# Performance work log

Measured on AMD Instinct MI355X. Metric: run time of the kernel, lower is better.

The kernel has to match this reference:

```python
import jax, jax.numpy as jnp
import numpy as np

CS = 64          # chunk_size
CP = CS - 1      # causal_padding
H = 8            # heads
DH = 64          # dim_head
SCALE = DH ** -0.5


def rotate_half(x):
    x1, x2 = jnp.split(x, 2, axis=-1)
    return jnp.concatenate((-x2, x1), axis=-1)


def apply_rope(t, freqs):
    rd = freqs.shape[-1]
    t_rot, t_pass = t[..., :rd], t[..., rd:]
    t_rot = t_rot * jnp.cos(freqs) + rotate_half(t_rot) * jnp.sin(freqs)
    return jnp.concatenate((t_rot, t_pass), axis=-1)


def setup_inputs() -> dict:
    key = jax.random.key(0)
    ks = jax.random.split(key, 10)
    b, n, dim = 4, 4096, 1024
    k_chunks, r, rlen = 64, 2, 128
    inner = H * DH
    return {
        "x": jax.random.normal(ks[0], (b, n, dim), dtype=jnp.float32),
        "context": jax.random.normal(ks[1], (b, k_chunks, r, rlen, dim), dtype=jnp.float32),
        "q_pos_emb": jax.random.normal(ks[2], (1, 1, CS, DH), dtype=jnp.float32),
        "k_pos_emb": jax.random.normal(ks[3], (1, 1, rlen, DH), dtype=jnp.float32),
        "Wq": jax.random.normal(ks[4], (dim, inner), dtype=jnp.float32) * 0.02,
        "Wk": jax.random.normal(ks[5], (dim, inner), dtype=jnp.float32) * 0.02,
        "Wv": jax.random.normal(ks[6], (dim, inner), dtype=jnp.float32) * 0.02,
        "Wo": jax.random.normal(ks[7], (inner, dim), dtype=jnp.float32) * 0.02,
        "bo": jnp.zeros((dim,), dtype=jnp.float32),
        "null_k": jax.random.normal(ks[8], (inner,), dtype=jnp.float32),
        "null_v": jax.random.normal(ks[9], (inner,), dtype=jnp.float32),
    }


def reference(x, context, q_pos_emb, k_pos_emb, Wq, Wk, Wv, Wo, bo, null_k, null_v):
    b, n, dim = x.shape
    _, k_chunks, r, rlen, _ = context.shape
    # causal shift: drop first CP tokens, pad CP zeros at end (F.pad with -CP)
    xs = jnp.pad(x[:, CP:], ((0, 0), (0, CP), (0, 0)))
    seq_index = (n // CS) * CS
    rem = n - seq_index
    xs = xs[:, :seq_index]                                   # [b, k*CS, dim]
    # shift q rope the same way; pad region gets freqs=0 -> identity rotation
    qpe = jnp.pad(q_pos_emb[:, :, CP:], ((0, 0), (0, 0), (0, CP), (0, 0)))
    kpe = jnp.tile(k_pos_emb, (1, 1, r, 1))                  # [1,1,r*rlen,DH]
    bk = b * k_chunks
    xc = xs.reshape(bk, CS, dim)
    ctx = context.reshape(bk, r * rlen, dim)
    # projections -> [bk, h, seq, dh]
    q = (xc @ Wq).reshape(bk, CS, H, DH).transpose(0, 2, 1, 3) * SCALE
    k = (ctx @ Wk).reshape(bk, r * rlen, H, DH).transpose(0, 2, 1, 3)
    v = (ctx @ Wv).reshape(bk, r * rlen, H, DH).transpose(0, 2, 1, 3)
    q = apply_rope(q, qpe)
    k = apply_rope(k, kpe)
    # null kv prepend
    nk = jnp.broadcast_to(null_k.reshape(1, H, 1, DH), (bk, H, 1, DH))
    nv = jnp.broadcast_to(null_v.reshape(1, H, 1, DH), (bk, H, 1, DH))
    k = jnp.concatenate((nk, k), axis=2)
    v = jnp.concatenate((nv, v), axis=2)
    sim = jnp.einsum('bhid,bhjd->bhij', q, k)
    attn = jax.nn.softmax(sim, axis=-1)
    o = jnp.einsum('bhij,bhjd->bhid', attn, v)
    o = o.transpose(0, 2, 1, 3).reshape(bk, CS, H * DH)
    o = o @ Wo + bo                                          # [bk, CS, dim]
    o = o.reshape(b, k_chunks * CS, dim)
    # unshift: pad CP zeros at front, trim CP - rem from end
    o = jnp.concatenate(
        (jnp.zeros((b, CP, dim), o.dtype), o[:, :k_chunks * CS - CP + rem]), axis=1)
    return o
```

## Files before the change

kernel.cpp:

```cpp
#include <hip/hip_runtime.h>


#define DEV __device__ __forceinline__

typedef __bf16 bf16x8 __attribute__((ext_vector_type(8)));
typedef float f32x4 __attribute__((ext_vector_type(4)));

DEV unsigned short f2bf(float f) {
  union { float f; unsigned int u; } v; v.f = f;
  unsigned int u = v.u;
  unsigned int r = (u + 0x7FFFu + ((u >> 16) & 1u)) >> 16;
  return (unsigned short)r;
}
DEV float bf2f(unsigned short h) {
  union { unsigned int u; float f; } v; v.u = ((unsigned int)h) << 16;
  return v.f;
}
DEV unsigned int pkbf(unsigned int hi, unsigned int lo) {
  return __builtin_amdgcn_perm(hi, lo, 0x07060302u);
}

DEV void ldst16(const void* g, void* l) {
  __builtin_amdgcn_global_load_lds(
      (const __attribute__((address_space(1))) void*)g,
      (__attribute__((address_space(3))) void*)l, 16, 0, 0);
}

__global__ __launch_bounds__(256) void prep_k(const float* __restrict__ Wq,
                                              const float* __restrict__ Wk,
                                              const float* __restrict__ Wv,
                                              const float* __restrict__ Wo,
                                              const float* __restrict__ qpe,
                                              const float* __restrict__ kpe,
                                              unsigned short* __restrict__ Wqt,
                                              unsigned short* __restrict__ Wkt,
                                              unsigned short* __restrict__ Wvt,
                                              unsigned short* __restrict__ Wot,
                                              float* __restrict__ ck, float* __restrict__ sk,
                                              float* __restrict__ cq, float* __restrict__ sq,
                                              float* __restrict__ out) {
  int blk = blockIdx.x;
  if (blk < 8192) {
    int idx = blk * 256 + threadIdx.x;
    int which = idx >> 19;
    int loc = idx & 524287;
    if (which < 3) {
      int k = loc & 1023, n = loc >> 10;
      const float* W = which == 0 ? Wq : (which == 1 ? Wk : Wv);
      unsigned short* Wt = which == 0 ? Wqt : (which == 1 ? Wkt : Wvt);
      float scale = which == 0 ? 0.125f : 1.0f;
      Wt[loc] = f2bf(W[(size_t)k * 512 + n] * scale);
    } else {
      int k = loc & 511, n = loc >> 9;
      Wot[loc] = f2bf(Wo[(size_t)k * 1024 + n]);
    }
  } else if (blk < 8444) {
    int r = blk - 8192;
    int b = r / 63, rr = r % 63;
    float4 z = {0.f, 0.f, 0.f, 0.f};
    *(float4*)(out + (((size_t)(b * 4096 + rr)) << 10) + threadIdx.x * 4) = z;
  } else {
    int t = (blk - 8444) * 256 + threadIdx.x;
    float f = kpe[t];
    ck[t] = cosf(f);
    sk[t] = sinf(f);
    if (t < 64) {
      float g = qpe[63 * 64 + t];
      cq[t] = cosf(g);
      sq[t] = sinf(g);
    }
  }
}

template <int MODE>
__global__ __launch_bounds__(256) void gemm_proj(const float* __restrict__ Af,
                                                 const unsigned short* __restrict__ B0,
                                                 const unsigned short* __restrict__ B1,
                                                 unsigned short* __restrict__ out0,
                                                 unsigned short* __restrict__ out1,
                                                 const float* __restrict__ ck,
                                                 const float* __restrict__ sk,
                                                 const float* __restrict__ cq,
                                                 const float* __restrict__ sq) {
  __shared__ unsigned short sh[16384];
  unsigned short* As = sh;
  unsigned short* Bs = sh + 8192;
  const int K = 1024;

  int id = blockIdx.x;
  int x, y, z;
  if (MODE == 0) { x = (id & 7) + 8 * (id >> 5); y = (id >> 3) & 3; z = 0; }
  else           { x = (id & 7) + 8 * (id >> 6); int j = (id >> 3) & 7; y = j & 3; z = j >> 2; }
  const unsigned short* B = z ? B1 : B0;
  int m0 = x * 128, n0 = y * 128;
  int tid = threadIdx.x, w = tid >> 6, lane = tid & 63;
  int wm = (w & 1) * 64, wn = (w >> 1) * 64;
  int Lrow = lane >> 3, Lc = lane & 7;
  int srcC = Lc ^ (Lrow & 7);

  const float* asrc[4];
  bool avalid[4];
  #pragma unroll
  for (int q = 0; q < 4; ++q) {
    int t = w * 4 + q;
    int gm = m0 + t * 8 + Lrow;
    if (MODE == 0) {
      int b = gm >> 12, p = gm & 4095;
      avalid[q] = (p <= 4032);
      asrc[q] = Af + (((size_t)(b << 12) + p + 63) << 10) + srcC * 8;
    } else {
      avalid[q] = true;
      asrc[q] = Af + (size_t)gm * 1024 + srcC * 8;
    }
  }

  f32x4 acc[4][4] = {};

  for (int k0 = 0; k0 < K; k0 += 64) {
    #pragma unroll
    for (int q = 0; q < 4; ++q) {
      int t = w * 4 + q;
      uint4 lo = {0, 0, 0, 0}, hi = {0, 0, 0, 0};
      if (avalid[q]) {
        lo = *(const uint4*)(asrc[q] + k0);
        hi = *(const uint4*)(asrc[q] + k0 + 4);
      }
      uint4 pk;
      pk.x = pkbf(lo.y, lo.x);
      pk.y = pkbf(lo.w, lo.z);
      pk.z = pkbf(hi.y, hi.x);
      pk.w = pkbf(hi.w, hi.z);
      *(uint4*)((char*)As + t * 1024 + lane * 16) = pk;
      ldst16(B + (size_t)(n0 + t * 8 + Lrow) * K + (k0 + srcC * 8), (char*)Bs + t * 1024);
    }
    __syncthreads();
    #pragma unroll
    for (int k32 = 0; k32 < 2; ++k32) {
      int c = k32 * 4 + (lane >> 4);
      bf16x8 af[4], bfr[4];
      #pragma unroll
      for (int mt = 0; mt < 4; ++mt) {
        int m = wm + mt * 16 + (lane & 15);
        af[mt] = *(const bf16x8*)((const char*)As + m * 128 + (c ^ (m & 7)) * 16);
      }
      #pragma unroll
      for (int nt = 0; nt < 4; ++nt) {
        int n = wn + nt * 16 + (lane & 15);
        bfr[nt] = *(const bf16x8*)((const char*)Bs + n * 128 + (c ^ (n & 7)) * 16);
      }
      #pragma unroll
      for (int mt = 0; mt < 4; ++mt)
        #pragma unroll
        for (int nt = 0; nt < 4; ++nt)
          acc[mt][nt] = __builtin_amdgcn_mfma_f32_16x16x32_bf16(af[mt], bfr[nt], acc[mt][nt], 0, 0, 0);
    }
    __syncthreads();
  }

  if (MODE == 0) {
    #pragma unroll
    for (int mt = 0; mt < 4; ++mt)
      #pragma unroll
      for (int nt = 0; nt < 4; ++nt)
        #pragma unroll
        for (int r = 0; r < 4; ++r) {
          int m = m0 + wm + mt * 16 + (lane >> 4) * 4 + r;
          int n = n0 + wn + nt * 16 + (lane & 15);
          float val = acc[mt][nt][r];
          if ((m & 63) == 0) {
            int d = nt * 16 + (lane & 15);
            float partner = acc[mt][nt ^ 2][r];
            val = val * cq[d] + (nt < 2 ? -partner : partner) * sq[d];
          }
          out0[(size_t)m * 512 + n] = f2bf(val);
        }
  } else if (z == 0) {
    #pragma unroll
    for (int mt = 0; mt < 4; ++mt)
      #pragma unroll
      for (int r = 0; r < 4; ++r) {
        int m = m0 + wm + mt * 16 + (lane >> 4) * 4 + r;
        int fib = (m & 127) * 64;
        #pragma unroll
        for (int nt = 0; nt < 4; ++nt) {
          int n = n0 + wn + nt * 16 + (lane & 15);
          int d = nt * 16 + (lane & 15);
          float partner = acc[mt][nt ^ 2][r];
          float val = acc[mt][nt][r] * ck[fib + d] + (nt < 2 ? -partner : partner) * sk[fib + d];
          out0[(size_t)m * 512 + n] = f2bf(val);
        }
      }
  } else {
    #pragma unroll
    for (int mt = 0; mt < 4; ++mt)
      #pragma unroll
      for (int nt = 0; nt < 4; ++nt)
        #pragma unroll
        for (int r = 0; r < 4; ++r) {
          int ml = wm + mt * 16 + (lane >> 4) * 4 + r;
          int nl = wn + nt * 16 + (lane & 15);
          int mc = ml >> 3, me = ml & 7;
          *(unsigned short*)((char*)sh + nl * 256 + ((mc ^ (nl & 15)) * 16) + me * 2) =
              f2bf(acc[mt][nt][r]);
        }
    __syncthreads();
    #pragma unroll
    for (int i = 0; i < 8; ++i) {
      int flat = i * 256 + tid;
      int nl = flat >> 4, mc = flat & 15;
      uint4 v = *(const uint4*)((const char*)sh + nl * 256 + ((mc ^ (nl & 15)) * 16));
      *(uint4*)(out1 + (size_t)(n0 + nl) * 65536 + m0 + mc * 8) = v;
    }
  }
}

__global__ __launch_bounds__(256) void gemm_out(const unsigned short* __restrict__ A,
                                                const unsigned short* __restrict__ B,
                                                const float* __restrict__ bias,
                                                float* __restrict__ out) {
  __shared__ unsigned short sh[16384];
  unsigned short* As = sh;
  unsigned short* Bs = sh + 8192;
  const int K = 512, N = 1024;
  int id = blockIdx.x;
  int x = (id & 7) + 8 * (id >> 6), y = (id >> 3) & 7;
  int m0 = x * 128, n0 = y * 128;
  int tid = threadIdx.x, w = tid >> 6, lane = tid & 63;
  int wm = (w & 1) * 64, wn = (w >> 1) * 64;
  int Lrow = lane >> 3, Lc = lane & 7;
  int srcC = Lc ^ (Lrow & 7);

  f32x4 acc[4][4] = {};

  for (int k0 = 0; k0 < K; k0 += 64) {
    #pragma unroll
    for (int q = 0; q < 4; ++q) {
      int t = w * 4 + q;
      ldst16(A + (size_t)(m0 + t * 8 + Lrow) * K + (k0 + srcC * 8), (char*)As + t * 1024);
      ldst16(B + (size_t)(n0 + t * 8 + Lrow) * K + (k0 + srcC * 8), (char*)Bs + t * 1024);
    }
    __syncthreads();
    #pragma unroll
    for (int k32 = 0; k32 < 2; ++k32) {
      int c = k32 * 4 + (lane >> 4);
      bf16x8 af[4], bfr[4];
      #pragma unroll
      for (int mt = 0; mt < 4; ++mt) {
        int m = wm + mt * 16 + (lane & 15);
        af[mt] = *(const bf16x8*)((const char*)As + m * 128 + (c ^ (m & 7)) * 16);
      }
      #pragma unroll
      for (int nt = 0; nt < 4; ++nt) {
        int n = wn + nt * 16 + (lane & 15);
        bfr[nt] = *(const bf16x8*)((const char*)Bs + n * 128 + (c ^ (n & 7)) * 16);
      }
      #pragma unroll
      for (int mt = 0; mt < 4; ++mt)
        #pragma unroll
        for (int nt = 0; nt < 4; ++nt)
          acc[mt][nt] = __builtin_amdgcn_mfma_f32_16x16x32_bf16(af[mt], bfr[nt], acc[mt][nt], 0, 0, 0);
    }
    __syncthreads();
  }
  #pragma unroll
  for (int mt = 0; mt < 4; ++mt)
    #pragma unroll
    for (int nt = 0; nt < 4; ++nt)
      #pragma unroll
      for (int r = 0; r < 4; ++r) {
        int m = m0 + wm + mt * 16 + (lane >> 4) * 4 + r;
        int n = n0 + wn + nt * 16 + (lane & 15);
        int b = m >> 12, t = m & 4095;
        if (t <= 4032)
          out[((size_t)((b << 12) + t + 63)) * N + n] = acc[mt][nt][r] + bias[n];
      }
}

__global__ __launch_bounds__(256) void attn_kernel(const unsigned short* __restrict__ qb,
                                                   const unsigned short* __restrict__ kb,
                                                   const unsigned short* __restrict__ vtg,
                                                   const float* __restrict__ nullk,
                                                   const float* __restrict__ nullv,
                                                   unsigned short* __restrict__ ob) {
  __shared__ unsigned short qs[64 * 64];
  __shared__ unsigned short ks[256 * 64];
  __shared__ unsigned short ps[64 * 256];
  __shared__ float rnull[64];
  __shared__ float rsum[64];
  int id = blockIdx.x;
  int bc = (id & 7) + 8 * (id >> 6);
  int h = (id >> 3) & 7;
  int tid = threadIdx.x, w = tid >> 6, lane = tid & 63;
  int Lrow = lane >> 3, Lc = lane & 7, srcC = Lc ^ (Lrow & 7);

  #pragma unroll
  for (int q8 = 0; q8 < 2; ++q8) {
    int t = w * 2 + q8;
    ldst16(qb + (size_t)(bc * 64 + t * 8 + Lrow) * 512 + h * 64 + srcC * 8, (char*)qs + t * 1024);
  }
  #pragma unroll
  for (int q8 = 0; q8 < 8; ++q8) {
    int t = w * 8 + q8;
    ldst16(kb + (size_t)(bc * 256 + t * 8 + Lrow) * 512 + h * 64 + srcC * 8, (char*)ks + t * 1024);
  }
  __syncthreads();

  {
    int rl = lane >> 2, part = lane & 3;
    int row = w * 16 + rl;
    float s = 0.f;
    #pragma unroll
    for (int e = 0; e < 16; ++e) {
      int d = part * 16 + e;
      unsigned short qv = *(const unsigned short*)((const char*)qs + row * 128 +
                                                   (((d >> 3) ^ (row & 7)) * 16) + (d & 7) * 2);
      s += bf2f(qv) * nullk[h * 64 + d];
    }
    s += __shfl_xor(s, 1);
    s += __shfl_xor(s, 2);
    if (part == 0) rnull[row] = __expf(s);
  }

  f32x4 acc[16] = {};
  #pragma unroll
  for (int k32 = 0; k32 < 2; ++k32) {
    int c = k32 * 4 + (lane >> 4);
    int m = w * 16 + (lane & 15);
    bf16x8 a = *(const bf16x8*)((const char*)qs + m * 128 + (c ^ (m & 7)) * 16);
    #pragma unroll
    for (int nt = 0; nt < 16; ++nt) {
      int n = nt * 16 + (lane & 15);
      bf16x8 b = *(const bf16x8*)((const char*)ks + n * 128 + (c ^ (n & 7)) * 16);
      acc[nt] = __builtin_amdgcn_mfma_f32_16x16x32_bf16(a, b, acc[nt], 0, 0, 0);
    }
  }

  int g = lane >> 4;
  #pragma unroll
  for (int r = 0; r < 4; ++r) {
    int row = w * 16 + g * 4 + r;
    float s = 0.f;
    #pragma unroll
    for (int nt = 0; nt < 16; ++nt) {
      float p = __expf(acc[nt][r]);
      acc[nt][r] = p;
      s += p;
    }
    s += __shfl_xor(s, 1);
    s += __shfl_xor(s, 2);
    s += __shfl_xor(s, 4);
    s += __shfl_xor(s, 8);
    if ((lane & 15) == 0) rsum[row] = s + rnull[row];
  }

  #pragma unroll
  for (int nt = 0; nt < 16; ++nt)
    #pragma unroll
    for (int r = 0; r < 4; ++r) {
      int row = w * 16 + g * 4 + r;
      int col = nt * 16 + (lane & 15);
      *(unsigned short*)((char*)ps + row * 512 + (((col >> 3) ^ (row & 7)) * 16) + (col & 7) * 2) =
          f2bf(acc[nt][r]);
    }
  __syncthreads();

  #pragma unroll
  for (int q8 = 0; q8 < 8; ++q8) {
    int t = w * 8 + q8;
    int dd = t * 2 + (lane >> 5);
    int cl = (lane & 31) ^ (dd & 7);
    ldst16(vtg + (size_t)(h * 64 + dd) * 65536 + bc * 256 + cl * 8, (char*)ks + t * 1024);
  }
  __syncthreads();

  f32x4 oacc[4] = {};
  #pragma unroll
  for (int k32 = 0; k32 < 8; ++k32) {
    int c = k32 * 4 + (lane >> 4);
    int m = w * 16 + (lane & 15);
    bf16x8 a = *(const bf16x8*)((const char*)ps + m * 512 + (c ^ (m & 7)) * 16);
    #pragma unroll
    for (int nt = 0; nt < 4; ++nt) {
      int n = nt * 16 + (lane & 15);
      bf16x8 b = *(const bf16x8*)((const char*)ks + n * 512 + (c ^ (n & 7)) * 16);
      oacc[nt] = __builtin_amdgcn_mfma_f32_16x16x32_bf16(a, b, oacc[nt], 0, 0, 0);
    }
  }
  #pragma unroll
  for (int nt = 0; nt < 4; ++nt)
    #pragma unroll
    for (int r = 0; r < 4; ++r) {
      int row = w * 16 + g * 4 + r;
      int d = nt * 16 + (lane & 15);
      float o = oacc[nt][r] + rnull[row] * nullv[h * 64 + d];
      o /= rsum[row];
      ob[((size_t)(bc * 64 + row) * 8 + h) * 64 + d] = f2bf(o);
    }
}

extern "C" void kernel_launch(void* const* d_in, const int* in_sizes, int n_in,
                              void* d_out, int out_size, void* d_ws, size_t ws_size,
                              hipStream_t stream) {
  const float* x = (const float*)d_in[0];
  const float* ctx = (const float*)d_in[1];
  const float* qpe = (const float*)d_in[2];
  const float* kpe = (const float*)d_in[3];
  const float* Wq = (const float*)d_in[4];
  const float* Wk = (const float*)d_in[5];
  const float* Wv = (const float*)d_in[6];
  const float* Wo = (const float*)d_in[7];
  const float* bo = (const float*)d_in[8];
  const float* nk = (const float*)d_in[9];
  const float* nv = (const float*)d_in[10];
  float* out = (float*)d_out;
  char* ws = (char*)d_ws;

  unsigned short* Wqt  = (unsigned short*)(ws + 0);
  unsigned short* Wkt  = (unsigned short*)(ws + 1048576);
  unsigned short* Wvt  = (unsigned short*)(ws + 2097152);
  unsigned short* Wot  = (unsigned short*)(ws + 3145728);
  unsigned short* qb   = (unsigned short*)(ws + 4194304);
  unsigned short* kb   = (unsigned short*)(ws + 20971520);
  unsigned short* vtg  = (unsigned short*)(ws + 88080384);
  unsigned short* obuf = (unsigned short*)(ws + 155189248);
  float* cosk = (float*)(ws + 171966464);
  float* sink = (float*)(ws + 171999232);
  float* cosq = (float*)(ws + 172032000);
  float* sinq = (float*)(ws + 172032256);

  prep_k<<<8476, 256, 0, stream>>>(Wq, Wk, Wv, Wo, qpe, kpe, Wqt, Wkt, Wvt, Wot,
                                   cosk, sink, cosq, sinq, out);

  gemm_proj<0><<<512, 256, 0, stream>>>(x, Wqt, Wqt, qb, nullptr,
                                        cosk, sink, cosq, sinq);
  gemm_proj<1><<<4096, 256, 0, stream>>>(ctx, Wkt, Wvt, kb, vtg,
                                         cosk, sink, cosq, sinq);

  attn_kernel<<<2048, 256, 0, stream>>>(qb, kb, vtg, nk, nv, obuf);

  gemm_out<<<1024, 256, 0, stream>>>(obuf, Wot, bo, out);
}
```

Before: 763.5 us.

## Add pipelined 256x256 KV projection GEMM and tiled weight transpose

Replaces the KV projection launch with a new gemm_kv kernel. It uses 512 threads and 256x256 tiles, double-buffered LDS, and register-staged fp32-to-bf16 conversion of the context input. Asynchronous global-to-LDS loads of B are interleaved with MFMA phases under explicit barriers, waitcnts and setprio. Separately, the weight transpose in prep_k now goes through a 64x64 shared-memory tile so both reads and writes are coalesced. The pipeline adds barrier overhead and a large LDS footprint, which limits occupancy.

```diff
diff --git a/kernel.cpp b/kernel.cpp
--- a/kernel.cpp
+++ b/kernel.cpp
@@ -25,6 +25,11 @@
       (const __attribute__((address_space(1))) void*)g,
       (__attribute__((address_space(3))) void*)l, 16, 0, 0);
 }
+
+DEV void bar() { __builtin_amdgcn_s_barrier(); }
+#define LGKM0 asm volatile("s_waitcnt lgkmcnt(0)" ::: "memory")
+#define VMCNT4 asm volatile("s_waitcnt vmcnt(4)" ::: "memory")
+#define VMCNT0 asm volatile("s_waitcnt vmcnt(0)" ::: "memory")
 
 __global__ __launch_bounds__(256) void prep_k(const float* __restrict__ Wq,
                                               const float* __restrict__ Wk,
@@ -39,28 +44,42 @@
                                               float* __restrict__ ck, float* __restrict__ sk,
                                               float* __restrict__ cq, float* __restrict__ sq,
                                               float* __restrict__ out) {
+  __shared__ float tl[64][65];
   int blk = blockIdx.x;
-  if (blk < 8192) {
-    int idx = blk * 256 + threadIdx.x;
-    int which = idx >> 19;
-    int loc = idx & 524287;
-    if (which < 3) {
-      int k = loc & 1023, n = loc >> 10;
-      const float* W = which == 0 ? Wq : (which == 1 ? Wk : Wv);
-      unsigned short* Wt = which == 0 ? Wqt : (which == 1 ? Wkt : Wvt);
-      float scale = which == 0 ? 0.125f : 1.0f;
-      Wt[loc] = f2bf(W[(size_t)k * 512 + n] * scale);
-    } else {
-      int k = loc & 511, n = loc >> 9;
-      Wot[loc] = f2bf(Wo[(size_t)k * 1024 + n]);
-    }
-  } else if (blk < 8444) {
-    int r = blk - 8192;
+  int tid = threadIdx.x;
+  if (blk < 512) {
+    int mat = blk >> 7, loc = blk & 127;
+    const float* W;
+    unsigned short* Wt;
+    int R, C;
+    float scale = 1.0f;
+    if (mat == 0)      { W = Wq; Wt = Wqt; R = 1024; C = 512; scale = 0.125f; }
+    else if (mat == 1) { W = Wk; Wt = Wkt; R = 1024; C = 512; }
+    else if (mat == 2) { W = Wv; Wt = Wvt; R = 1024; C = 512; }
+    else               { W = Wo; Wt = Wot; R = 512;  C = 1024; }
+    int nct = C >> 6;
+    int rt = loc / nct, ct = loc % nct;
+    int r0 = rt << 6, c0 = ct << 6;
+    #pragma unroll
+    for (int i = 0; i < 16; ++i) {
+      int flat = i * 256 + tid;
+      int rr = flat >> 6, cc = flat & 63;
+      tl[rr][cc] = W[(size_t)(r0 + rr) * C + c0 + cc] * scale;
+    }
+    __syncthreads();
+    #pragma unroll
+    for (int i = 0; i < 16; ++i) {
+      int flat = i * 256 + tid;
+      int cc = flat >> 6, rr = flat & 63;
+      Wt[(size_t)(c0 + cc) * R + r0 + rr] = f2bf(tl[rr][cc]);
+    }
+  } else if (blk < 764) {
+    int r = blk - 512;
     int b = r / 63, rr = r % 63;
     float4 z = {0.f, 0.f, 0.f, 0.f};
-    *(float4*)(out + (((size_t)(b * 4096 + rr)) << 10) + threadIdx.x * 4) = z;
+    *(float4*)(out + (((size_t)(b * 4096 + rr)) << 10) + tid * 4) = z;
   } else {
-    int t = (blk - 8444) * 256 + threadIdx.x;
+    int t = (blk - 764) * 256 + tid;
     float f = kpe[t];
     ck[t] = cosf(f);
     sk[t] = sinf(f);
@@ -210,6 +229,214 @@
       int nl = flat >> 4, mc = flat & 15;
       uint4 v = *(const uint4*)((const char*)sh + nl * 256 + ((mc ^ (nl & 15)) * 16));
       *(uint4*)(out1 + (size_t)(n0 + nl) * 65536 + m0 + mc * 8) = v;
+    }
+  }
+}
+
+DEV bf16x8 rdfrag(const unsigned short* b, int row, int c) {
+  return *(const bf16x8*)((const char*)b + row * 128 + ((c ^ (row & 7)) << 4));
+}
+
+DEV void rdA(const unsigned short* bufA, int wm, int ln15, int l4, int mtb,
+             bf16x8 (&af)[2][2]) {
+  #pragma unroll
+  for (int mq = 0; mq < 2; ++mq)
+    #pragma unroll
+    for (int kk = 0; kk < 2; ++kk)
+      af[mq][kk] = rdfrag(bufA, wm + (mtb + mq) * 16 + ln15, kk * 4 + l4);
+}
+
+DEV void rdB(const unsigned short* bufB, int wn, int ln15, int l4, bf16x8 (&bf)[4][2]) {
+  #pragma unroll
+  for (int nt = 0; nt < 4; ++nt)
+    #pragma unroll
+    for (int kk = 0; kk < 2; ++kk)
+      bf[nt][kk] = rdfrag(bufB, wn + nt * 16 + ln15, kk * 4 + l4);
+}
+
+template <int MTB>
+DEV void mfma16(const bf16x8 (&af)[2][2], const bf16x8 (&bf)[4][2], f32x4 (&acc)[8][4]) {
+  __builtin_amdgcn_s_setprio(1);
+  #pragma unroll
+  for (int mq = 0; mq < 2; ++mq)
+    #pragma unroll
+    for (int nt = 0; nt < 4; ++nt)
+      #pragma unroll
+      for (int kk = 0; kk < 2; ++kk)
+        acc[MTB + mq][nt] = __builtin_amdgcn_mfma_f32_16x16x32_bf16(
+            af[mq][kk], bf[nt][kk], acc[MTB + mq][nt], 0, 0, 0);
+  __builtin_amdgcn_s_setprio(0);
+}
+
+DEV void aload(const float* Af, int m0, int rowt, int csrc, int k0, uint4 (&al)[8]) {
+  #pragma unroll
+  for (int q = 0; q < 4; ++q) {
+    const float* s = Af + (size_t)(m0 + q * 64 + rowt) * 1024 + k0 + csrc * 8;
+    al[2 * q] = *(const uint4*)s;
+    al[2 * q + 1] = *(const uint4*)(s + 4);
+  }
+}
+
+DEV void apack(unsigned short* bufA, int tid, const uint4 (&al)[8]) {
+  #pragma unroll
+  for (int q = 0; q < 4; ++q) {
+    uint4 pk;
+    pk.x = pkbf(al[2 * q].y, al[2 * q].x);
+    pk.y = pkbf(al[2 * q].w, al[2 * q].z);
+    pk.z = pkbf(al[2 * q + 1].y, al[2 * q + 1].x);
+    pk.w = pkbf(al[2 * q + 1].w, al[2 * q + 1].z);
+    *(uint4*)((char*)bufA + ((q * 512 + tid) << 4)) = pk;
+  }
+}
+
+DEV void bstage(unsigned short* bufB, const unsigned short* Bsrc, int n0, int w,
+                int Lrow, int srcC, int k0, int h) {
+  #pragma unroll
+  for (int qq = 0; qq < 2; ++qq) {
+    int q = 2 * h + qq;
+    ldst16(Bsrc + (size_t)(n0 + q * 64 + w * 8 + Lrow) * 1024 + k0 + srcC * 8,
+           (char*)bufB + ((q * 512 + w * 64) << 4));
+  }
+}
+
+__global__ __launch_bounds__(512, 2) void gemm_kv(const float* __restrict__ Af,
+                                                  const unsigned short* __restrict__ Bk,
+                                                  const unsigned short* __restrict__ Bv,
+                                                  unsigned short* __restrict__ kb,
+                                                  unsigned short* __restrict__ vtg,
+                                                  const float* __restrict__ ck,
+                                                  const float* __restrict__ sk) {
+  __shared__ unsigned short sh[65536];
+  unsigned short* A0b = sh;
+  unsigned short* A1b = sh + 16384;
+  unsigned short* B0b = sh + 32768;
+  unsigned short* B1b = sh + 49152;
+
+  int id = blockIdx.x;
+  int x = (id & 7) + 8 * (id >> 5);
+  int j = (id >> 3) & 3;
+  int y = j & 1, z = j >> 1;
+  const unsigned short* Bz = z ? Bv : Bk;
+  int m0 = x << 8, n0 = y << 8;
+
+  int tid = threadIdx.x, w = tid >> 6, lane = tid & 63;
+  int wm = (w & 1) * 128, wn = (w >> 1) * 64;
+  int ln15 = lane & 15, l4 = lane >> 4;
+  int Lrow = lane >> 3;
+  int srcC = (lane & 7) ^ (Lrow & 7);
+  int rowt = tid >> 3;
+  int csrc = (tid & 7) ^ (rowt & 7);
+
+  f32x4 acc[8][4] = {};
+  uint4 al[8];
+
+  aload(Af, m0, rowt, csrc, 0, al);
+  bstage(B0b, Bz, n0, w, Lrow, srcC, 0, 0);
+  bstage(B0b, Bz, n0, w, Lrow, srcC, 0, 1);
+  bstage(B1b, Bz, n0, w, Lrow, srcC, 64, 0);
+  bstage(B1b, Bz, n0, w, Lrow, srcC, 64, 1);
+  apack(A0b, tid, al);
+  LGKM0;
+  VMCNT4;
+  bar();
+
+  for (int it = 0; it < 8; ++it) {
+    const int k0a = it * 128;
+    bf16x8 af[2][2], bf[4][2];
+
+    rdB(B0b, wn, ln15, l4, bf);
+    rdA(A0b, wm, ln15, l4, 0, af);
+    aload(Af, m0, rowt, csrc, k0a + 64, al);
+    bar();
+    mfma16<0>(af, bf, acc);
+    bar();
+
+    rdA(A0b, wm, ln15, l4, 2, af);
+    bar();
+    mfma16<2>(af, bf, acc);
+    bar();
+
+    rdA(A0b, wm, ln15, l4, 4, af);
+    bstage(B0b, Bz, n0, w, Lrow, srcC, (k0a + 128) & 1023, 0);
+    bar();
+    mfma16<4>(af, bf, acc);
+    bar();
+
+    rdA(A0b, wm, ln15, l4, 6, af);
+    bstage(B0b, Bz, n0, w, Lrow, srcC, (k0a + 128) & 1023, 1);
+    apack(A1b, tid, al);
+    LGKM0;
+    VMCNT4;
+    bar();
+    mfma16<6>(af, bf, acc);
+    bar();
+
+    rdB(B1b, wn, ln15, l4, bf);
+    rdA(A1b, wm, ln15, l4, 0, af);
+    aload(Af, m0, rowt, csrc, (k0a + 128) & 1023, al);
+    bar();
+    mfma16<0>(af, bf, acc);
+    bar();
+
+    rdA(A1b, wm, ln15, l4, 2, af);
+    bar();
+    mfma16<2>(af, bf, acc);
+    bar();
+
+    rdA(A1b, wm, ln15, l4, 4, af);
+    bstage(B1b, Bz, n0, w, Lrow, srcC, (k0a + 192) & 1023, 0);
+    bar();
+    mfma16<4>(af, bf, acc);
+    bar();
+
+    rdA(A1b, wm, ln15, l4, 6, af);
+    bstage(B1b, Bz, n0, w, Lrow, srcC, (k0a + 192) & 1023, 1);
+    apack(A0b, tid, al);
+    LGKM0;
+    VMCNT4;
+    bar();
+    mfma16<6>(af, bf, acc);
+    bar();
+  }
+
+  VMCNT0;
+  bar();
+
+  if (z == 0) {
+    #pragma unroll
+    for (int mt = 0; mt < 8; ++mt)
+      #pragma unroll
+      for (int r = 0; r < 4; ++r) {
+        int m = m0 + wm + mt * 16 + l4 * 4 + r;
+        int fib = (m & 127) << 6;
+        #pragma unroll
+        for (int nt = 0; nt < 4; ++nt) {
+          int d = nt * 16 + ln15;
+          float partner = acc[mt][nt ^ 2][r];
+          float val = acc[mt][nt][r] * ck[fib + d] + (nt < 2 ? -partner : partner) * sk[fib + d];
+          kb[(size_t)m * 512 + n0 + wn + d] = f2bf(val);
+        }
+      }
+  } else {
+    #pragma unroll
+    for (int mt = 0; mt < 8; ++mt)
+      #pragma unroll
+      for (int nt = 0; nt < 4; ++nt)
+        #pragma unroll
+        for (int r = 0; r < 4; ++r) {
+          int ml = wm + mt * 16 + l4 * 4 + r;
+          int nl = wn + nt * 16 + ln15;
+          int mc = ml >> 3, me = ml & 7;
+          *(unsigned short*)((char*)sh + nl * 512 + ((mc ^ (nl & 31)) << 4) + me * 2) =
+              f2bf(acc[mt][nt][r]);
+        }
+    __syncthreads();
+    #pragma unroll
+    for (int i = 0; i < 16; ++i) {
+      int flat = i * 512 + tid;
+      int nl = flat >> 5, mc = flat & 31;
+      uint4 v = *(const uint4*)((const char*)sh + nl * 512 + ((mc ^ (nl & 31)) << 4));
+      *(uint4*)(vtg + (size_t)(n0 + nl) * 65536 + m0 + mc * 8) = v;
     }
   }
 }
@@ -428,13 +655,12 @@
   float* cosq = (float*)(ws + 172032000);
   float* sinq = (float*)(ws + 172032256);
 
-  prep_k<<<8476, 256, 0, stream>>>(Wq, Wk, Wv, Wo, qpe, kpe, Wqt, Wkt, Wvt, Wot,
-                                   cosk, sink, cosq, sinq, out);
+  prep_k<<<796, 256, 0, stream>>>(Wq, Wk, Wv, Wo, qpe, kpe, Wqt, Wkt, Wvt, Wot,
+                                  cosk, sink, cosq, sinq, out);
 
   gemm_proj<0><<<512, 256, 0, stream>>>(x, Wqt, Wqt, qb, nullptr,
                                         cosk, sink, cosq, sinq);
-  gemm_proj<1><<<4096, 256, 0, stream>>>(ctx, Wkt, Wvt, kb, vtg,
-                                         cosk, sink, cosq, sinq);
+  gemm_kv<<<1024, 512, 0, stream>>>(ctx, Wkt, Wvt, kb, vtg, cosk, sink);
 
   attn_kernel<<<2048, 256, 0, stream>>>(qb, kb, vtg, nk, nv, obuf);
 
```

Result: faster. 707.2 us (-7.4%).
